# Performance work log

Hardware: AMD Instinct MI355X
Metric: run time of the kernel (lower is better)

The kernel has to match this reference:

```python
import jax, jax.numpy as jnp
import numpy as np
from jax import lax

B = 1024
LATENT = 512          # latent_dim (must equal conductor_output_dim, see forward feedback)
COND_H = 1024         # conductor_hidden_size
COND_OUT = 512        # conductor_output_dim
BOT_H = 1024          # bottom_decoder_hidden_size
OUT = 90              # output_size
NUM_SUB = 16          # hardcoded outer steps
SUB_LEN = 4           # hardcoded inner steps


def setup_inputs() -> dict:
    key = jax.random.key(0)
    ks = jax.random.split(key, 32)
    p = lambda k, shape: (jax.random.normal(k, shape, jnp.float32) * 0.02)
    bot_in = COND_OUT + OUT  # 602
    return {
        "z": jax.random.normal(ks[0], (B, LATENT), jnp.float32),
        "input_sequence": jax.random.uniform(ks[1], (B, NUM_SUB, SUB_LEN, OUT), jnp.float32),
        # fc_z
        "fc_z_w": p(ks[2], (COND_H, LATENT)), "fc_z_b": p(ks[3], (COND_H,)),
        # conductor LSTM (2 layers, torch gate order i,f,g,o)
        "cWih0": p(ks[4], (4 * COND_H, LATENT)), "cWhh0": p(ks[5], (4 * COND_H, COND_H)),
        "cbih0": p(ks[6], (4 * COND_H,)), "cbhh0": p(ks[7], (4 * COND_H,)),
        "cWih1": p(ks[8], (4 * COND_H, COND_H)), "cWhh1": p(ks[9], (4 * COND_H, COND_H)),
        "cbih1": p(ks[10], (4 * COND_H,)), "cbhh1": p(ks[11], (4 * COND_H,)),
        # fc_1 and conductor_fc
        "fc1_w": p(ks[12], (COND_OUT, COND_H)), "fc1_b": p(ks[13], (COND_OUT,)),
        "cfc_w": p(ks[14], (COND_OUT, COND_OUT)), "cfc_b": p(ks[15], (COND_OUT,)),
        # bottom decoder LSTM (2 layers)
        "bWih0": p(ks[16], (4 * BOT_H, bot_in)), "bWhh0": p(ks[17], (4 * BOT_H, BOT_H)),
        "bbih0": p(ks[18], (4 * BOT_H,)), "bbhh0": p(ks[19], (4 * BOT_H,)),
        "bWih1": p(ks[20], (4 * BOT_H, BOT_H)), "bWhh1": p(ks[21], (4 * BOT_H, BOT_H)),
        "bbih1": p(ks[22], (4 * BOT_H,)), "bbhh1": p(ks[23], (4 * BOT_H,)),
        # output layer
        "out_w": p(ks[24], (OUT, BOT_H)), "out_b": p(ks[25], (OUT,)),
    }


def _lstm_cell(x, h, c, Wih, Whh, bih, bhh):
    # torch LSTM cell: gates in i,f,g,o order
    gates = x @ Wih.T + bih + h @ Whh.T + bhh
    i, f, g, o = jnp.split(gates, 4, axis=-1)
    c_new = jax.nn.sigmoid(f) * c + jax.nn.sigmoid(i) * jnp.tanh(g)
    h_new = jax.nn.sigmoid(o) * jnp.tanh(c_new)
    return h_new, c_new


def reference(z, input_sequence, fc_z_w, fc_z_b,
              cWih0, cWhh0, cbih0, cbhh0, cWih1, cWhh1, cbih1, cbhh1,
              fc1_w, fc1_b, cfc_w, cfc_b,
              bWih0, bWhh0, bbih0, bbhh0, bWih1, bWhh1, bbih1, bbhh1,
              out_w, out_b):
    bsz = z.shape[0]
    out_dim = out_b.shape[0]
    bot_h = bWhh0.shape[1]

    # initial conductor state: tanh(fc_z(z)) used as (h, c) for both layers
    s0 = jnp.tanh(z @ fc_z_w.T + fc_z_b)  # [B, COND_H]
    cond_in0 = jnp.zeros((bsz, z.shape[1]), z.dtype)  # zeros(latent_dim)
    prev0 = jnp.zeros((bsz, out_dim), z.dtype)

    def outer(carry, _):
        cond_in, h1, c1, h2, c2, prev = carry
        h1, c1 = _lstm_cell(cond_in, h1, c1, cWih0, cWhh0, cbih0, cbhh0)
        h2, c2 = _lstm_cell(h1, h2, c2, cWih1, cWhh1, cbih1, cbhh1)
        cond_out = h2 @ fc1_w.T + fc1_b                    # [B, COND_OUT]
        emb = jnp.tanh(cond_out @ cfc_w.T + cfc_b)         # same every inner step
        z0 = jnp.zeros((bsz, bot_h), z.dtype)              # bottom state reset each subsequence

        def inner(ic, _):
            bh1, bc1, bh2, bc2, p = ic
            x = jnp.concatenate([emb, p], axis=1)          # [B, COND_OUT + OUT]
            bh1, bc1 = _lstm_cell(x, bh1, bc1, bWih0, bWhh0, bbih0, bbhh0)
            bh2, bc2 = _lstm_cell(bh1, bh2, bc2, bWih1, bWhh1, bbih1, bbhh1)
            p = bh2 @ out_w.T + out_b                      # [B, OUT]
            return (bh1, bc1, bh2, bc2, p), p

        (_, _, _, _, prev_last), ys = lax.scan(inner, (z0, z0, z0, z0, prev), None, length=SUB_LEN)
        # conductor_input for next step is fc_1 output (feedback in original code)
        return (cond_out, h1, c1, h2, c2, prev_last), ys   # ys: [SUB_LEN, B, OUT]

    _, outs = lax.scan(outer, (cond_in0, s0, s0, s0, s0, prev0), None, length=NUM_SUB)
    # outs: [NUM_SUB, SUB_LEN, B, OUT] -> [B, NUM_SUB*SUB_LEN, OUT]
    out = outs.reshape(NUM_SUB * SUB_LEN, bsz, out_dim).transpose(1, 0, 2)
    return jax.nn.sigmoid(out)
```

## Files before the change

### kernel.cpp

```cpp
#include <hip/hip_runtime.h>
#include <cstdint>
#include <cstddef>

typedef unsigned short u16;
typedef unsigned int u32;
typedef float f32x4 __attribute__((ext_vector_type(4)));
typedef _Float16 f16x8 __attribute__((ext_vector_type(8)));

__device__ __forceinline__ u16 f2h(float x) {
  _Float16 h = (_Float16)x;
  return __builtin_bit_cast(u16, h);
}
__device__ __forceinline__ float sigm(float x) { return 1.f / (1.f + __expf(-x)); }

__device__ __forceinline__ void gll16(const void* g, void* l) {
  __builtin_amdgcn_global_load_lds(
      (const __attribute__((address_space(1))) void*)g,
      (__attribute__((address_space(3))) void*)l, 16, 0, 0);
}

enum { M_PLAIN = 0, M_TANH = 1, M_OUT = 2 };

struct GemmP {
  const u16* A; int lda;
  const u16* W; int ldw;
  int K;
  const float* bias;
  int mode;
  int czero;
  u16* d0; int ld0;
  u16* d1; int ld1;
  float* c0;
  float* c1;
  float* fout;
};

template <bool CELL>
__global__ __launch_bounds__(512, 2) void gk(GemmP p) {
  __shared__ __align__(16) char sm[131072];
  const int tid = threadIdx.x;
  const int lane = tid & 63, wid = tid >> 6;
  const int wr = wid >> 1, wc = wid & 1;
  int bx, by;
  if (CELL) {
    const int hw = blockIdx.x;
    const int xcd = hw & 7, idx = hw >> 3;
    by = xcd * 4 + (idx >> 3);
    bx = idx & 7;
  } else {
    bx = blockIdx.x;
    by = blockIdx.y;
  }
  const int bRow = bx * 128;
  const int nBase = by * (CELL ? 32 : 128);
  const int col0 = lane & 15, g4 = lane >> 4;

  f32x4 acc[2][4];
#pragma unroll
  for (int m = 0; m < 2; ++m)
#pragma unroll
    for (int n = 0; n < 4; ++n) acc[m][n] = f32x4{0.f, 0.f, 0.f, 0.f};

  const char* Ab = (const char*)p.A;
  const char* Wb = (const char*)p.W;
  const size_t ldaB = (size_t)p.lda * 2, ldwB = (size_t)p.ldw * 2;

  auto stage = [&](int buf, int kt) {
    char* base = sm + buf * 32768;
    const int kb = kt * 128;
#pragma unroll
    for (int i = 0; i < 2; ++i) {
      const int s = i * 512 + tid;
      const int row = s >> 3, ch = s & 7;
      const int sch = ch ^ (row & 7);
      gll16(Ab + (size_t)(bRow + row) * ldaB + (size_t)(kb + sch * 16),
            base + s * 16);
      const int wrow = CELL ? ((row >> 5) * 1024 + nBase + (row & 31)) : (nBase + row);
      gll16(Wb + (size_t)wrow * ldwB + (size_t)(kb + sch * 16),
            base + 16384 + s * 16);
    }
  };

  const int nt = p.K >> 6;
  stage(0, 0);
  stage(1, 1);
  for (int t = 0; t < nt; ++t) {
    if (t + 2 < nt) stage((t + 2) & 3, t + 2);
    const int ahead = (nt - 1 - t < 2) ? (nt - 1 - t) : 2;
    if (ahead == 2)      asm volatile("s_waitcnt vmcnt(8)" ::: "memory");
    else if (ahead == 1) asm volatile("s_waitcnt vmcnt(4)" ::: "memory");
    else                 asm volatile("s_waitcnt vmcnt(0)" ::: "memory");
    __builtin_amdgcn_s_barrier();

    const char* Abase = sm + (t & 3) * 32768;
    const char* Wbase = Abase + 16384;
    f16x8 af[2][2], wf[2][4];
#pragma unroll
    for (int kf = 0; kf < 2; ++kf) {
      const int ch = kf * 4 + g4;
#pragma unroll
      for (int m = 0; m < 2; ++m) {
        const int r = wr * 32 + m * 16 + col0;
        af[kf][m] = *(const f16x8*)(Abase + r * 128 + ((ch ^ (r & 7)) << 4));
      }
#pragma unroll
      for (int n = 0; n < 4; ++n) {
        const int r = CELL ? (n * 32 + wc * 16 + col0) : (wc * 64 + n * 16 + col0);
        wf[kf][n] = *(const f16x8*)(Wbase + r * 128 + ((ch ^ (r & 7)) << 4));
      }
    }
#pragma unroll
    for (int kf = 0; kf < 2; ++kf)
#pragma unroll
      for (int m = 0; m < 2; ++m)
#pragma unroll
        for (int n = 0; n < 4; ++n)
          acc[m][n] = __builtin_amdgcn_mfma_f32_16x16x32_f16(af[kf][m], wf[kf][n],
                                                             acc[m][n], 0, 0, 0);
  }

  if (CELL) {
    const int j = nBase + wc * 16 + col0;
    const float bi = p.bias[j], bf_ = p.bias[j + 1024];
    const float bg = p.bias[j + 2048], bo = p.bias[j + 3072];
#pragma unroll
    for (int m = 0; m < 2; ++m) {
#pragma unroll
      for (int r = 0; r < 4; ++r) {
        const int b = bRow + wr * 32 + m * 16 + g4 * 4 + r;
        const float gi = acc[m][0][r] + bi;
        const float gf = acc[m][1][r] + bf_;
        const float gg = acc[m][2][r] + bg;
        const float go = acc[m][3][r] + bo;
        const size_t ci = (size_t)b * 1024 + j;
        const float cprev = p.czero ? 0.f : p.c0[ci];
        const float cn = sigm(gf) * cprev + sigm(gi) * tanhf(gg);
        p.c0[ci] = cn;
        const u16 hv = f2h(sigm(go) * tanhf(cn));
        p.d0[(size_t)b * p.ld0 + j] = hv;
        if (p.d1) p.d1[(size_t)b * p.ld1 + j] = hv;
      }
    }
  } else {
#pragma unroll
    for (int m = 0; m < 2; ++m)
#pragma unroll
      for (int n = 0; n < 4; ++n)
#pragma unroll
        for (int r = 0; r < 4; ++r) {
          const int b = bRow + wr * 32 + m * 16 + g4 * 4 + r;
          const int j = nBase + wc * 64 + n * 16 + col0;
          float v = acc[m][n][r] + p.bias[j];
          if (p.mode == M_TANH) {
            v = tanhf(v);
            const u16 hv = f2h(v);
            p.d0[(size_t)b * p.ld0 + j] = hv;
            if (p.d1) p.d1[(size_t)b * p.ld1 + j] = hv;
            if (p.c0) p.c0[(size_t)b * 1024 + j] = v;
            if (p.c1) p.c1[(size_t)b * 1024 + j] = v;
          } else if (p.mode == M_PLAIN) {
            p.d0[(size_t)b * p.ld0 + j] = f2h(v);
          } else {
            if (j < 90) {
              p.d0[(size_t)b * p.ld0 + j] = f2h(v);
              p.fout[(size_t)b * 5760 + j] = sigm(v);
            }
          }
        }
  }
}


__global__ void pack_w(u16* dst, const float* a, int Ka, const float* b, int Kb,
                       int gap, int Kp, int srcRows) {
  const int r = blockIdx.y;
  const int c = blockIdx.x * 256 + threadIdx.x;
  if (c >= Kp) return;
  float v = 0.f;
  if (r < srcRows) {
    if (c < Ka) v = a[(size_t)r * Ka + c];
    else if (c >= Ka + gap && c < Ka + gap + Kb) v = b[(size_t)r * Kb + (c - Ka - gap)];
  }
  dst[(size_t)r * Kp + c] = f2h(v);
}

struct BiasAll {
  float *bz, *bc0, *bc1, *bfc1, *bcfc, *bb0, *bb1, *bout;
  const float *fzb, *ci0, *ch0, *ci1, *ch1, *f1b, *cfb, *bi0, *bh0, *bi1, *bh1, *ob;
};
__global__ void pack_biases(BiasAll q) {
  int i = blockIdx.x * 256 + threadIdx.x;
  if (i < 1024) { q.bz[i] = q.fzb[i]; return; } i -= 1024;
  if (i < 4096) { q.bc0[i] = q.ci0[i] + q.ch0[i]; return; } i -= 4096;
  if (i < 4096) { q.bc1[i] = q.ci1[i] + q.ch1[i]; return; } i -= 4096;
  if (i < 512)  { q.bfc1[i] = q.f1b[i]; return; } i -= 512;
  if (i < 512)  { q.bcfc[i] = q.cfb[i]; return; } i -= 512;
  if (i < 4096) { q.bb0[i] = q.bi0[i] + q.bh0[i]; return; } i -= 4096;
  if (i < 4096) { q.bb1[i] = q.bi1[i] + q.bh1[i]; return; } i -= 4096;
  if (i < 128)  { q.bout[i] = (i < 90) ? q.ob[i] : 0.f; }
}

__global__ void conv_h(u16* dst, const float* src, long n) {
  for (long i = (long)blockIdx.x * blockDim.x + threadIdx.x; i < n;
       i += (long)gridDim.x * blockDim.x)
    dst[i] = f2h(src[i]);
}

__global__ void zero_init(u32* xc0, u32* xb0) {
  const int i = blockIdx.x * 256 + threadIdx.x;
  if (i < 1024 * 256) {
    xc0[(i >> 8) * 768 + (i & 255)] = 0;
  } else {
    const int k = i - 1024 * 256;
    xb0[(k >> 6) * 832 + 256 + (k & 63)] = 0;
  }
}

extern "C" void kernel_launch(void* const* d_in, const int* in_sizes, int n_in,
                              void* d_out, int out_size, void* d_ws, size_t ws_size,
                              hipStream_t stream) {
  const float* z      = (const float*)d_in[0];
  const float* fc_z_w = (const float*)d_in[2];
  const float* fc_z_b = (const float*)d_in[3];
  const float* cWih0  = (const float*)d_in[4];
  const float* cWhh0  = (const float*)d_in[5];
  const float* cbih0  = (const float*)d_in[6];
  const float* cbhh0  = (const float*)d_in[7];
  const float* cWih1  = (const float*)d_in[8];
  const float* cWhh1  = (const float*)d_in[9];
  const float* cbih1  = (const float*)d_in[10];
  const float* cbhh1  = (const float*)d_in[11];
  const float* fc1_w  = (const float*)d_in[12];
  const float* fc1_b  = (const float*)d_in[13];
  const float* cfc_w  = (const float*)d_in[14];
  const float* cfc_b  = (const float*)d_in[15];
  const float* bWih0  = (const float*)d_in[16];
  const float* bWhh0  = (const float*)d_in[17];
  const float* bbih0  = (const float*)d_in[18];
  const float* bbhh0  = (const float*)d_in[19];
  const float* bWih1  = (const float*)d_in[20];
  const float* bWhh1  = (const float*)d_in[21];
  const float* bbih1  = (const float*)d_in[22];
  const float* bbhh1  = (const float*)d_in[23];
  const float* out_w  = (const float*)d_in[24];
  const float* out_b  = (const float*)d_in[25];
  float* outp = (float*)d_out;

  char* w = (char*)d_ws;
  auto alloc = [&](size_t bytes) {
    char* p = w;
    w += (bytes + 255) & ~(size_t)255;
    return p;
  };
  u16* Wz   = (u16*)alloc((size_t)1024 * 512 * 2);
  u16* Wc0  = (u16*)alloc((size_t)4096 * 1536 * 2);
  u16* Wc1  = (u16*)alloc((size_t)4096 * 2048 * 2);
  u16* Wb0  = (u16*)alloc((size_t)4096 * 1664 * 2);
  u16* Wb1  = (u16*)alloc((size_t)4096 * 2048 * 2);
  u16* Wfc1 = (u16*)alloc((size_t)512 * 1024 * 2);
  u16* Wcfc = (u16*)alloc((size_t)512 * 512 * 2);
  u16* Wout = (u16*)alloc((size_t)128 * 1024 * 2);
  u16* zh   = (u16*)alloc((size_t)1024 * 512 * 2);
  u16* Xc0  = (u16*)alloc((size_t)1024 * 1536 * 2);
  u16* Xc1  = (u16*)alloc((size_t)1024 * 2048 * 2);
  u16* Xb0  = (u16*)alloc((size_t)1024 * 1664 * 2);
  u16* Xb1  = (u16*)alloc((size_t)1024 * 2048 * 2);
  float* cc0  = (float*)alloc((size_t)1024 * 1024 * 4);
  float* cc1  = (float*)alloc((size_t)1024 * 1024 * 4);
  float* cbb0 = (float*)alloc((size_t)1024 * 1024 * 4);
  float* cbb1 = (float*)alloc((size_t)1024 * 1024 * 4);
  float* bz   = (float*)alloc(1024 * 4);
  float* bc0  = (float*)alloc(4096 * 4);
  float* bc1  = (float*)alloc(4096 * 4);
  float* bfc1 = (float*)alloc(512 * 4);
  float* bcfc = (float*)alloc(512 * 4);
  float* bb0  = (float*)alloc(4096 * 4);
  float* bb1  = (float*)alloc(4096 * 4);
  float* bout = (float*)alloc(128 * 4);

  const dim3 blk(256), blk5(512);
  const dim3 gcell(256);

  pack_w<<<dim3(2, 1024), blk, 0, stream>>>(Wz,   fc_z_w, 512,  nullptr, 0,    0,  512,  1024);
  pack_w<<<dim3(6, 4096), blk, 0, stream>>>(Wc0,  cWih0,  512,  cWhh0,   1024, 0,  1536, 4096);
  pack_w<<<dim3(8, 4096), blk, 0, stream>>>(Wc1,  cWih1,  1024, cWhh1,   1024, 0,  2048, 4096);
  pack_w<<<dim3(7, 4096), blk, 0, stream>>>(Wb0,  bWih0,  602,  bWhh0,   1024, 38, 1664, 4096);
  pack_w<<<dim3(8, 4096), blk, 0, stream>>>(Wb1,  bWih1,  1024, bWhh1,   1024, 0,  2048, 4096);
  pack_w<<<dim3(4, 512),  blk, 0, stream>>>(Wfc1, fc1_w,  1024, nullptr, 0,    0,  1024, 512);
  pack_w<<<dim3(2, 512),  blk, 0, stream>>>(Wcfc, cfc_w,  512,  nullptr, 0,    0,  512,  512);
  pack_w<<<dim3(4, 128),  blk, 0, stream>>>(Wout, out_w,  1024, nullptr, 0,    0,  1024, 90);
  {
    BiasAll q{bz, bc0, bc1, bfc1, bcfc, bb0, bb1, bout,
              fc_z_b, cbih0, cbhh0, cbih1, cbhh1, fc1_b, cfc_b,
              bbih0, bbhh0, bbih1, bbhh1, out_b};
    pack_biases<<<dim3(80), blk, 0, stream>>>(q);
  }
  conv_h<<<dim3(512), blk, 0, stream>>>(zh, z, 1024L * 512);
  zero_init<<<dim3(1280), blk, 0, stream>>>((u32*)Xc0, (u32*)Xb0);

  {
    GemmP p;
    p.A = zh; p.lda = 512; p.W = Wz; p.ldw = 512; p.K = 512; p.bias = bz;
    p.mode = M_TANH; p.czero = 0;
    p.d0 = Xc0 + 512; p.ld0 = 1536; p.d1 = Xc1 + 1024; p.ld1 = 2048;
    p.c0 = cc0; p.c1 = cc1; p.fout = nullptr;
    gk<false><<<dim3(8, 8), blk5, 0, stream>>>(p);
  }

  for (int t = 0; t < 16; ++t) {
    {
      GemmP p;
      p.A = Xc0; p.lda = 1536; p.W = Wc0; p.ldw = 1536; p.K = 1536; p.bias = bc0;
      p.mode = 0; p.czero = 0;
      p.d0 = Xc0 + 512; p.ld0 = 1536; p.d1 = Xc1; p.ld1 = 2048;
      p.c0 = cc0; p.c1 = nullptr; p.fout = nullptr;
      gk<true><<<gcell, blk5, 0, stream>>>(p);
    }
    {
      GemmP p;
      p.A = Xc1; p.lda = 2048; p.W = Wc1; p.ldw = 2048; p.K = 2048; p.bias = bc1;
      p.mode = 0; p.czero = 0;
      p.d0 = Xc1 + 1024; p.ld0 = 2048; p.d1 = nullptr; p.ld1 = 0;
      p.c0 = cc1; p.c1 = nullptr; p.fout = nullptr;
      gk<true><<<gcell, blk5, 0, stream>>>(p);
    }
    {
      GemmP p;
      p.A = Xc1 + 1024; p.lda = 2048; p.W = Wfc1; p.ldw = 1024; p.K = 1024;
      p.bias = bfc1; p.mode = M_PLAIN; p.czero = 0;
      p.d0 = Xc0; p.ld0 = 1536; p.d1 = nullptr; p.ld1 = 0;
      p.c0 = nullptr; p.c1 = nullptr; p.fout = nullptr;
      gk<false><<<dim3(8, 4), blk5, 0, stream>>>(p);
    }
    {
      GemmP p;
      p.A = Xc0; p.lda = 1536; p.W = Wcfc; p.ldw = 512; p.K = 512;
      p.bias = bcfc; p.mode = M_TANH; p.czero = 0;
      p.d0 = Xb0; p.ld0 = 1664; p.d1 = nullptr; p.ld1 = 0;
      p.c0 = nullptr; p.c1 = nullptr; p.fout = nullptr;
      gk<false><<<dim3(8, 4), blk5, 0, stream>>>(p);
    }
    for (int s = 0; s < 4; ++s) {
      {
        GemmP p;
        p.A = Xb0; p.lda = 1664; p.W = Wb0; p.ldw = 1664;
        p.K = (s == 0) ? 640 : 1664; p.bias = bb0;
        p.mode = 0; p.czero = (s == 0);
        p.d0 = Xb0 + 640; p.ld0 = 1664; p.d1 = Xb1; p.ld1 = 2048;
        p.c0 = cbb0; p.c1 = nullptr; p.fout = nullptr;
        gk<true><<<gcell, blk5, 0, stream>>>(p);
      }
      {
        GemmP p;
        p.A = Xb1; p.lda = 2048; p.W = Wb1; p.ldw = 2048;
        p.K = (s == 0) ? 1024 : 2048; p.bias = bb1;
        p.mode = 0; p.czero = (s == 0);
        p.d0 = Xb1 + 1024; p.ld0 = 2048; p.d1 = nullptr; p.ld1 = 0;
        p.c0 = cbb1; p.c1 = nullptr; p.fout = nullptr;
        gk<true><<<gcell, blk5, 0, stream>>>(p);
      }
      {
        GemmP p;
        p.A = Xb1 + 1024; p.lda = 2048; p.W = Wout; p.ldw = 1024; p.K = 1024;
        p.bias = bout; p.mode = M_OUT; p.czero = 0;
        p.d0 = Xb0 + 512; p.ld0 = 1664; p.d1 = nullptr; p.ld1 = 0;
        p.c0 = nullptr; p.c1 = nullptr;
        p.fout = outp + (size_t)(t * 4 + s) * 90;
        gk<false><<<dim3(8, 1), blk5, 0, stream>>>(p);
      }
    }
  }
}
```

Before: 5.003 ms.

## Fold conductor_fc into fc_1 via precomputed weight product; use 256-thread blocks

```diff
diff --git a/kernel.cpp b/kernel.cpp
--- a/kernel.cpp
+++ b/kernel.cpp
@@ -19,7 +19,7 @@
       (__attribute__((address_space(3))) void*)l, 16, 0, 0);
 }
 
-enum { M_PLAIN = 0, M_TANH = 1, M_OUT = 2 };
+enum { M_PLAIN = 0, M_TANH = 1, M_OUT = 2, M_FC2 = 3 };
 
 struct GemmP {
   const u16* A; int lda;
@@ -36,7 +36,7 @@
 };
 
 template <bool CELL>
-__global__ __launch_bounds__(512, 2) void gk(GemmP p) {
+__global__ __launch_bounds__(256, 1) void gk(GemmP p) {
   __shared__ __align__(16) char sm[131072];
   const int tid = threadIdx.x;
   const int lane = tid & 63, wid = tid >> 6;
@@ -55,9 +55,9 @@
   const int nBase = by * (CELL ? 32 : 128);
   const int col0 = lane & 15, g4 = lane >> 4;
 
-  f32x4 acc[2][4];
-#pragma unroll
-  for (int m = 0; m < 2; ++m)
+  f32x4 acc[4][4];
+#pragma unroll
+  for (int m = 0; m < 4; ++m)
 #pragma unroll
     for (int n = 0; n < 4; ++n) acc[m][n] = f32x4{0.f, 0.f, 0.f, 0.f};
 
@@ -69,12 +69,18 @@
     char* base = sm + buf * 32768;
     const int kb = kt * 128;
 #pragma unroll
-    for (int i = 0; i < 2; ++i) {
-      const int s = i * 512 + tid;
+    for (int i = 0; i < 4; ++i) {
+      const int s = i * 256 + tid;
       const int row = s >> 3, ch = s & 7;
       const int sch = ch ^ (row & 7);
       gll16(Ab + (size_t)(bRow + row) * ldaB + (size_t)(kb + sch * 16),
             base + s * 16);
+    }
+#pragma unroll
+    for (int i = 0; i < 4; ++i) {
+      const int s = i * 256 + tid;
+      const int row = s >> 3, ch = s & 7;
+      const int sch = ch ^ (row & 7);
       const int wrow = CELL ? ((row >> 5) * 1024 + nBase + (row & 31)) : (nBase + row);
       gll16(Wb + (size_t)wrow * ldwB + (size_t)(kb + sch * 16),
             base + 16384 + s * 16);
@@ -87,20 +93,20 @@
   for (int t = 0; t < nt; ++t) {
     if (t + 2 < nt) stage((t + 2) & 3, t + 2);
     const int ahead = (nt - 1 - t < 2) ? (nt - 1 - t) : 2;
-    if (ahead == 2)      asm volatile("s_waitcnt vmcnt(8)" ::: "memory");
-    else if (ahead == 1) asm volatile("s_waitcnt vmcnt(4)" ::: "memory");
+    if (ahead == 2)      asm volatile("s_waitcnt vmcnt(16)" ::: "memory");
+    else if (ahead == 1) asm volatile("s_waitcnt vmcnt(8)" ::: "memory");
     else                 asm volatile("s_waitcnt vmcnt(0)" ::: "memory");
     __builtin_amdgcn_s_barrier();
 
     const char* Abase = sm + (t & 3) * 32768;
     const char* Wbase = Abase + 16384;
-    f16x8 af[2][2], wf[2][4];
+    f16x8 af[2][4], wf[2][4];
 #pragma unroll
     for (int kf = 0; kf < 2; ++kf) {
       const int ch = kf * 4 + g4;
 #pragma unroll
-      for (int m = 0; m < 2; ++m) {
-        const int r = wr * 32 + m * 16 + col0;
+      for (int m = 0; m < 4; ++m) {
+        const int r = wr * 64 + m * 16 + col0;
         af[kf][m] = *(const f16x8*)(Abase + r * 128 + ((ch ^ (r & 7)) << 4));
       }
 #pragma unroll
@@ -112,7 +118,7 @@
 #pragma unroll
     for (int kf = 0; kf < 2; ++kf)
 #pragma unroll
-      for (int m = 0; m < 2; ++m)
+      for (int m = 0; m < 4; ++m)
 #pragma unroll
         for (int n = 0; n < 4; ++n)
           acc[m][n] = __builtin_amdgcn_mfma_f32_16x16x32_f16(af[kf][m], wf[kf][n],
@@ -124,10 +130,10 @@
     const float bi = p.bias[j], bf_ = p.bias[j + 1024];
     const float bg = p.bias[j + 2048], bo = p.bias[j + 3072];
 #pragma unroll
-    for (int m = 0; m < 2; ++m) {
+    for (int m = 0; m < 4; ++m) {
 #pragma unroll
       for (int r = 0; r < 4; ++r) {
-        const int b = bRow + wr * 32 + m * 16 + g4 * 4 + r;
+        const int b = bRow + wr * 64 + m * 16 + g4 * 4 + r;
         const float gi = acc[m][0][r] + bi;
         const float gf = acc[m][1][r] + bf_;
         const float gg = acc[m][2][r] + bg;
@@ -143,12 +149,12 @@
     }
   } else {
 #pragma unroll
-    for (int m = 0; m < 2; ++m)
+    for (int m = 0; m < 4; ++m)
 #pragma unroll
       for (int n = 0; n < 4; ++n)
 #pragma unroll
         for (int r = 0; r < 4; ++r) {
-          const int b = bRow + wr * 32 + m * 16 + g4 * 4 + r;
+          const int b = bRow + wr * 64 + m * 16 + g4 * 4 + r;
           const int j = nBase + wc * 64 + n * 16 + col0;
           float v = acc[m][n][r] + p.bias[j];
           if (p.mode == M_TANH) {
@@ -160,6 +166,9 @@
             if (p.c1) p.c1[(size_t)b * 1024 + j] = v;
           } else if (p.mode == M_PLAIN) {
             p.d0[(size_t)b * p.ld0 + j] = f2h(v);
+          } else if (p.mode == M_FC2) {
+            if (j < 512) p.d0[(size_t)b * p.ld0 + j] = f2h(v);
+            else         p.d1[(size_t)b * p.ld1 + (j - 512)] = f2h(tanhf(v));
           } else {
             if (j < 90) {
               p.d0[(size_t)b * p.ld0 + j] = f2h(v);
@@ -184,20 +193,34 @@
   dst[(size_t)r * Kp + c] = f2h(v);
 }
 
+__global__ void pack_fc1T(u16* dst, const float* src) {
+  const int idx = blockIdx.x * 256 + threadIdx.x;
+  const int n = idx >> 9, j = idx & 511;
+  dst[idx] = f2h(src[(size_t)j * 1024 + n]);
+}
+
+__global__ void bias_fused(float* bfc2, const float* cfc_w, const float* fc1_b,
+                           const float* cfc_b) {
+  const int i = threadIdx.x;
+  float s = cfc_b[i];
+  for (int k = 0; k < 512; ++k) s += cfc_w[(size_t)i * 512 + k] * fc1_b[k];
+  bfc2[512 + i] = s;
+}
+
 struct BiasAll {
-  float *bz, *bc0, *bc1, *bfc1, *bcfc, *bb0, *bb1, *bout;
-  const float *fzb, *ci0, *ch0, *ci1, *ch1, *f1b, *cfb, *bi0, *bh0, *bi1, *bh1, *ob;
+  float *bz, *bc0, *bc1, *bfc2, *bb0, *bb1, *bout, *bzero;
+  const float *fzb, *ci0, *ch0, *ci1, *ch1, *f1b, *bi0, *bh0, *bi1, *bh1, *ob;
 };
 __global__ void pack_biases(BiasAll q) {
   int i = blockIdx.x * 256 + threadIdx.x;
   if (i < 1024) { q.bz[i] = q.fzb[i]; return; } i -= 1024;
   if (i < 4096) { q.bc0[i] = q.ci0[i] + q.ch0[i]; return; } i -= 4096;
   if (i < 4096) { q.bc1[i] = q.ci1[i] + q.ch1[i]; return; } i -= 4096;
-  if (i < 512)  { q.bfc1[i] = q.f1b[i]; return; } i -= 512;
-  if (i < 512)  { q.bcfc[i] = q.cfb[i]; return; } i -= 512;
+  if (i < 512)  { q.bfc2[i] = q.f1b[i]; return; } i -= 512;
   if (i < 4096) { q.bb0[i] = q.bi0[i] + q.bh0[i]; return; } i -= 4096;
   if (i < 4096) { q.bb1[i] = q.bi1[i] + q.bh1[i]; return; } i -= 4096;
-  if (i < 128)  { q.bout[i] = (i < 90) ? q.ob[i] : 0.f; }
+  if (i < 128)  { q.bout[i] = (i < 90) ? q.ob[i] : 0.f; return; } i -= 128;
+  if (i < 1024) { q.bzero[i] = 0.f; }
 }
 
 __global__ void conv_h(u16* dst, const float* src, long n) {
@@ -252,19 +275,20 @@
     w += (bytes + 255) & ~(size_t)255;
     return p;
   };
-  u16* Wz   = (u16*)alloc((size_t)1024 * 512 * 2);
-  u16* Wc0  = (u16*)alloc((size_t)4096 * 1536 * 2);
-  u16* Wc1  = (u16*)alloc((size_t)4096 * 2048 * 2);
-  u16* Wb0  = (u16*)alloc((size_t)4096 * 1664 * 2);
-  u16* Wb1  = (u16*)alloc((size_t)4096 * 2048 * 2);
-  u16* Wfc1 = (u16*)alloc((size_t)512 * 1024 * 2);
-  u16* Wcfc = (u16*)alloc((size_t)512 * 512 * 2);
-  u16* Wout = (u16*)alloc((size_t)128 * 1024 * 2);
-  u16* zh   = (u16*)alloc((size_t)1024 * 512 * 2);
-  u16* Xc0  = (u16*)alloc((size_t)1024 * 1536 * 2);
-  u16* Xc1  = (u16*)alloc((size_t)1024 * 2048 * 2);
-  u16* Xb0  = (u16*)alloc((size_t)1024 * 1664 * 2);
-  u16* Xb1  = (u16*)alloc((size_t)1024 * 2048 * 2);
+  u16* Wz    = (u16*)alloc((size_t)1024 * 512 * 2);
+  u16* Wc0   = (u16*)alloc((size_t)4096 * 1536 * 2);
+  u16* Wc1   = (u16*)alloc((size_t)4096 * 2048 * 2);
+  u16* Wb0   = (u16*)alloc((size_t)4096 * 1664 * 2);
+  u16* Wb1   = (u16*)alloc((size_t)4096 * 2048 * 2);
+  u16* Wfc2  = (u16*)alloc((size_t)1024 * 1024 * 2);
+  u16* Wcfc  = (u16*)alloc((size_t)512 * 512 * 2);
+  u16* fc1T  = (u16*)alloc((size_t)1024 * 512 * 2);
+  u16* Wout  = (u16*)alloc((size_t)128 * 1024 * 2);
+  u16* zh    = (u16*)alloc((size_t)1024 * 512 * 2);
+  u16* Xc0   = (u16*)alloc((size_t)1024 * 1536 * 2);
+  u16* Xc1   = (u16*)alloc((size_t)1024 * 2048 * 2);
+  u16* Xb0   = (u16*)alloc((size_t)1024 * 1664 * 2);
+  u16* Xb1   = (u16*)alloc((size_t)1024 * 2048 * 2);
   float* cc0  = (float*)alloc((size_t)1024 * 1024 * 4);
   float* cc1  = (float*)alloc((size_t)1024 * 1024 * 4);
   float* cbb0 = (float*)alloc((size_t)1024 * 1024 * 4);
@@ -272,13 +296,13 @@
   float* bz   = (float*)alloc(1024 * 4);
   float* bc0  = (float*)alloc(4096 * 4);
   float* bc1  = (float*)alloc(4096 * 4);
-  float* bfc1 = (float*)alloc(512 * 4);
-  float* bcfc = (float*)alloc(512 * 4);
+  float* bfc2 = (float*)alloc(1024 * 4);
   float* bb0  = (float*)alloc(4096 * 4);
   float* bb1  = (float*)alloc(4096 * 4);
   float* bout = (float*)alloc(128 * 4);
-
-  const dim3 blk(256), blk5(512);
+  float* bzero= (float*)alloc(1024 * 4);
+
+  const dim3 blk(256);
   const dim3 gcell(256);
 
   pack_w<<<dim3(2, 1024), blk, 0, stream>>>(Wz,   fc_z_w, 512,  nullptr, 0,    0,  512,  1024);
@@ -286,17 +310,27 @@
   pack_w<<<dim3(8, 4096), blk, 0, stream>>>(Wc1,  cWih1,  1024, cWhh1,   1024, 0,  2048, 4096);
   pack_w<<<dim3(7, 4096), blk, 0, stream>>>(Wb0,  bWih0,  602,  bWhh0,   1024, 38, 1664, 4096);
   pack_w<<<dim3(8, 4096), blk, 0, stream>>>(Wb1,  bWih1,  1024, bWhh1,   1024, 0,  2048, 4096);
-  pack_w<<<dim3(4, 512),  blk, 0, stream>>>(Wfc1, fc1_w,  1024, nullptr, 0,    0,  1024, 512);
+  pack_w<<<dim3(4, 512),  blk, 0, stream>>>(Wfc2, fc1_w,  1024, nullptr, 0,    0,  1024, 512);
   pack_w<<<dim3(2, 512),  blk, 0, stream>>>(Wcfc, cfc_w,  512,  nullptr, 0,    0,  512,  512);
   pack_w<<<dim3(4, 128),  blk, 0, stream>>>(Wout, out_w,  1024, nullptr, 0,    0,  1024, 90);
+  pack_fc1T<<<dim3(2048), blk, 0, stream>>>(fc1T, fc1_w);
   {
-    BiasAll q{bz, bc0, bc1, bfc1, bcfc, bb0, bb1, bout,
-              fc_z_b, cbih0, cbhh0, cbih1, cbhh1, fc1_b, cfc_b,
+    BiasAll q{bz, bc0, bc1, bfc2, bb0, bb1, bout, bzero,
+              fc_z_b, cbih0, cbhh0, cbih1, cbhh1, fc1_b,
               bbih0, bbhh0, bbih1, bbhh1, out_b};
     pack_biases<<<dim3(80), blk, 0, stream>>>(q);
   }
+  bias_fused<<<dim3(1), dim3(512), 0, stream>>>(bfc2, cfc_w, fc1_b, cfc_b);
   conv_h<<<dim3(512), blk, 0, stream>>>(zh, z, 1024L * 512);
   zero_init<<<dim3(1280), blk, 0, stream>>>((u32*)Xc0, (u32*)Xb0);
+  {
+    GemmP p;
+    p.A = Wcfc; p.lda = 512; p.W = fc1T; p.ldw = 512; p.K = 512; p.bias = bzero;
+    p.mode = M_PLAIN; p.czero = 0;
+    p.d0 = Wfc2 + (size_t)512 * 1024; p.ld0 = 1024; p.d1 = nullptr; p.ld1 = 0;
+    p.c0 = nullptr; p.c1 = nullptr; p.fout = nullptr;
+    gk<false><<<dim3(4, 8), blk, 0, stream>>>(p);
+  }
 
   {
     GemmP p;
@@ -304,7 +338,7 @@
     p.mode = M_TANH; p.czero = 0;
     p.d0 = Xc0 + 512; p.ld0 = 1536; p.d1 = Xc1 + 1024; p.ld1 = 2048;
     p.c0 = cc0; p.c1 = cc1; p.fout = nullptr;
-    gk<false><<<dim3(8, 8), blk5, 0, stream>>>(p);
+    gk<false><<<dim3(8, 8), blk, 0, stream>>>(p);
   }
 
   for (int t = 0; t < 16; ++t) {
@@ -314,7 +348,7 @@
       p.mode = 0; p.czero = 0;
       p.d0 = Xc0 + 512; p.ld0 = 1536; p.d1 = Xc1; p.ld1 = 2048;
       p.c0 = cc0; p.c1 = nullptr; p.fout = nullptr;
-      gk<true><<<gcell, blk5, 0, stream>>>(p);
+      gk<true><<<gcell, blk, 0, stream>>>(p);
     }
     {
       GemmP p;
@@ -322,23 +356,15 @@
       p.mode = 0; p.czero = 0;
       p.d0 = Xc1 + 1024; p.ld0 = 2048; p.d1 = nullptr; p.ld1 = 0;
       p.c0 = cc1; p.c1 = nullptr; p.fout = nullptr;
-      gk<true><<<gcell, blk5, 0, stream>>>(p);
+      gk<true><<<gcell, blk, 0, stream>>>(p);
     }
     {
       GemmP p;
-      p.A = Xc1 + 1024; p.lda = 2048; p.W = Wfc1; p.ldw = 1024; p.K = 1024;
-      p.bias = bfc1; p.mode = M_PLAIN; p.czero = 0;
-      p.d0 = Xc0; p.ld0 = 1536; p.d1 = nullptr; p.ld1 = 0;
+      p.A = Xc1 + 1024; p.lda = 2048; p.W = Wfc2; p.ldw = 1024; p.K = 1024;
+      p.bias = bfc2; p.mode = M_FC2; p.czero = 0;
+      p.d0 = Xc0; p.ld0 = 1536; p.d1 = Xb0; p.ld1 = 1664;
       p.c0 = nullptr; p.c1 = nullptr; p.fout = nullptr;
-      gk<false><<<dim3(8, 4), blk5, 0, stream>>>(p);
-    }
-    {
-      GemmP p;
-      p.A = Xc0; p.lda = 1536; p.W = Wcfc; p.ldw = 512; p.K = 512;
-      p.bias = bcfc; p.mode = M_TANH; p.czero = 0;
-      p.d0 = Xb0; p.ld0 = 1664; p.d1 = nullptr; p.ld1 = 0;
-      p.c0 = nullptr; p.c1 = nullptr; p.fout = nullptr;
-      gk<false><<<dim3(8, 4), blk5, 0, stream>>>(p);
+      gk<false><<<dim3(8, 8), blk, 0, stream>>>(p);
     }
     for (int s = 0; s < 4; ++s) {
       {
@@ -348,7 +374,7 @@
         p.mode = 0; p.czero = (s == 0);
         p.d0 = Xb0 + 640; p.ld0 = 1664; p.d1 = Xb1; p.ld1 = 2048;
         p.c0 = cbb0; p.c1 = nullptr; p.fout = nullptr;
-        gk<true><<<gcell, blk5, 0, stream>>>(p);
+        gk<true><<<gcell, blk, 0, stream>>>(p);
       }
       {
         GemmP p;
@@ -357,7 +383,7 @@
         p.mode = 0; p.czero = (s == 0);
         p.d0 = Xb1 + 1024; p.ld0 = 2048; p.d1 = nullptr; p.ld1 = 0;
         p.c0 = cbb1; p.c1 = nullptr; p.fout = nullptr;
-        gk<true><<<gcell, blk5, 0, stream>>>(p);
+        gk<true><<<gcell, blk, 0, stream>>>(p);
       }
       {
         GemmP p;
@@ -366,8 +392,8 @@
         p.d0 = Xb0 + 512; p.ld0 = 1664; p.d1 = nullptr; p.ld1 = 0;
         p.c0 = nullptr; p.c1 = nullptr;
         p.fout = outp + (size_t)(t * 4 + s) * 90;
-        gk<false><<<dim3(8, 1), blk5, 0, stream>>>(p);
-      }
-    }
-  }
-}
+        gk<false><<<dim3(8, 1), blk, 0, stream>>>(p);
+      }
+    }
+  }
+}
```

Result: slower. 6.632 ms (+32.6%).
